# Optimization experiments

Measured on AMD Instinct MI355X. Metric: run time of the kernel, lower is better.

Reference implementation:

```python
import jax, jax.numpy as jnp
import numpy as np

B, S, D, H = 2, 2048, 512, 8
HD = D // H  # head_dim = 64
LN_EPS = 1e-5


def setup_inputs() -> dict:
    key = jax.random.key(0)
    ks = jax.random.split(key, 12)
    sc = 1.0 / np.sqrt(D)
    inp = {
        'q': jax.random.normal(ks[0], (B, S, D), jnp.float32),
        'k': jax.random.normal(ks[1], (B, S, D), jnp.float32),
        'v': jax.random.normal(ks[2], (B, S, D), jnp.float32),
        # torch.nn.Linear stores weight as [out, in]; y = x @ W.T + b
        'wq': jax.random.normal(ks[3], (D, D), jnp.float32) * sc,
        'bq': jnp.zeros((D,), jnp.float32),
        'wk': jax.random.normal(ks[4], (D, D), jnp.float32) * sc,
        'bk': jnp.zeros((D,), jnp.float32),
        'wv': jax.random.normal(ks[5], (D, D), jnp.float32) * sc,
        'bv': jnp.zeros((D,), jnp.float32),
        'wo': jax.random.normal(ks[6], (D, D), jnp.float32) * sc,
        'bo': jnp.zeros((D,), jnp.float32),
        'gamma': jnp.ones((D,), jnp.float32),
        'beta': jnp.zeros((D,), jnp.float32),
        # causal mask: True above the diagonal -> filled with -inf
        'mask': jnp.broadcast_to(jnp.triu(jnp.ones((S, S), bool), k=1)[None, None], (B, 1, S, S)),
    }
    return inp


def _split_heads(x):
    # [B,S,D] -> [B,H,S,HD]
    return x.reshape(B, S, H, HD).transpose(0, 2, 1, 3)


def reference(q, k, v, wq, bq, wk, bk, wv, bv, wo, bo, gamma, beta, mask):
    residual = q
    Q = _split_heads(q @ wq.T + bq)
    K = _split_heads(k @ wk.T + bk)
    V = _split_heads(v @ wv.T + bv)
    scale = jnp.sqrt(jnp.float32(HD)) + 1e-8
    score = jnp.einsum('bhqd,bhkd->bhqk', Q, K) / scale
    score = jnp.where(mask, -jnp.inf, score)
    attn = jax.nn.softmax(score, axis=-1)
    ctx = jnp.einsum('bhqk,bhkd->bhqd', attn, V)
    ctx = ctx.transpose(0, 2, 1, 3).reshape(B, S, D)  # merge heads
    o = ctx @ wo.T + bo  # dropout is identity in eval mode
    x = residual + o
    mu = jnp.mean(x, axis=-1, keepdims=True)
    var = jnp.mean(jnp.square(x - mu), axis=-1, keepdims=True)
    return gamma * (x - mu) * jax.lax.rsqrt(var + LN_EPS) + beta
```

## Files before the change

### kernel.cpp

```cpp
#include <hip/hip_runtime.h>
#include <hip/hip_bf16.h>
#include <math.h>

#define BB 2
#define SS 2048
#define DD 512
#define HH 8
#define HD 64
#define LN_EPS 1e-5f

typedef _Float16 f16;
typedef f16 half8 __attribute__((ext_vector_type(8)));
typedef f16 half4 __attribute__((ext_vector_type(4)));
typedef __fp16 fp16x2 __attribute__((ext_vector_type(2)));

typedef float f32x4 __attribute__((ext_vector_type(4)));

__device__ __forceinline__ half4 cvt4(const float4 v) {
    const fp16x2 p0 = __builtin_amdgcn_cvt_pkrtz(v.x, v.y);
    const fp16x2 p1 = __builtin_amdgcn_cvt_pkrtz(v.z, v.w);
    half4 h;
    h.x = (f16)p0.x; h.y = (f16)p0.y; h.z = (f16)p1.x; h.w = (f16)p1.y;
    return h;
}

__global__ __launch_bounds__(128) void gemm_qkv(
    const float* __restrict__ qin, const float* __restrict__ kin,
    const float* __restrict__ vin,
    const float* __restrict__ wq, const float* __restrict__ wk,
    const float* __restrict__ wv,
    const float* __restrict__ bq, const float* __restrict__ bk,
    const float* __restrict__ bv,
    f16* __restrict__ Qh, f16* __restrict__ Kh, f16* __restrict__ Vt) {
    __shared__ f16 As[128][72];
    __shared__ f16 Bs[64][72];

    const int z = blockIdx.z;
    const float* A;  const float* W;  const float* bias;  f16* out;
    if (z == 0)      { A = qin; W = wq; bias = bq; out = Qh; }
    else if (z == 1) { A = kin; W = wk; bias = bk; out = Kh; }
    else             { A = vin; W = wv; bias = bv; out = Vt; }

    const int tid = threadIdx.x;
    const int lane = tid & 63;
    const int wid = tid >> 6;
    const int m0 = blockIdx.y * 128;
    const int n0 = blockIdx.x * 64;

    const int lr = tid >> 4;
    const int lc = (tid & 15) * 4;

    const int cl = lane & 15;
    const int g  = lane >> 4;

    f32x4 acc[4][4] = {};

    for (int k0 = 0; k0 < DD; k0 += 64) {
#pragma unroll
        for (int p = 0; p < 16; ++p) {
            const int r = p * 8 + lr;
            const float4 v = *reinterpret_cast<const float4*>(A + (size_t)(m0 + r) * DD + k0 + lc);
            *reinterpret_cast<half4*>(&As[r][lc]) = cvt4(v);
        }
#pragma unroll
        for (int p = 0; p < 8; ++p) {
            const int r = p * 8 + lr;
            const float4 v = *reinterpret_cast<const float4*>(W + (size_t)(n0 + r) * DD + k0 + lc);
            *reinterpret_cast<half4*>(&Bs[r][lc]) = cvt4(v);
        }
        __syncthreads();

#pragma unroll
        for (int ks = 0; ks < 2; ++ks) {
            const int co = ks * 32 + g * 8;
            half8 a[4], b[4];
#pragma unroll
            for (int i = 0; i < 4; ++i)
                a[i] = *reinterpret_cast<const half8*>(&As[wid * 64 + i * 16 + cl][co]);
#pragma unroll
            for (int j = 0; j < 4; ++j)
                b[j] = *reinterpret_cast<const half8*>(&Bs[j * 16 + cl][co]);
#pragma unroll
            for (int i = 0; i < 4; ++i)
#pragma unroll
                for (int j = 0; j < 4; ++j)
                    acc[i][j] = __builtin_amdgcn_mfma_f32_16x16x32_f16(a[i], b[j], acc[i][j], 0, 0, 0);
        }
        __syncthreads();
    }

    const int h = n0 >> 6;
#pragma unroll
    for (int i = 0; i < 4; ++i) {
#pragma unroll
        for (int r = 0; r < 4; ++r) {
            const int m = m0 + wid * 64 + i * 16 + g * 4 + r;
            const int b = m >> 11;
            const int s = m & (SS - 1);
#pragma unroll
            for (int j = 0; j < 4; ++j) {
                const int n = n0 + j * 16 + cl;
                const f16 y = (f16)(acc[i][j][r] + bias[n]);
                if (z == 2)
                    out[(((size_t)b * HH + h) * HD + (n & 63)) * SS + s] = y;
                else
                    out[(((size_t)b * HH + h) * SS + s) * HD + (n & 63)] = y;
            }
        }
    }
}

__global__ __launch_bounds__(256) void flash_f16(const f16* __restrict__ Qh,
                                                 const f16* __restrict__ Kh,
                                                 const f16* __restrict__ Vt,
                                                 float* __restrict__ Oc) {
    __shared__ f16 Ks[128][72];
    __shared__ f16 Vs[64][136];
    __shared__ f16 Ps[4][16][136];

    const int tid = threadIdx.x;
    const int lane = tid & 63;
    const int w = tid >> 6;
    const int qt = blockIdx.x;
    const int bh = blockIdx.y;
    const int cl = lane & 15;
    const int g  = lane >> 4;

    const f16* Qb = Qh + (size_t)bh * SS * HD;
    const f16* Kb = Kh + (size_t)bh * SS * HD;
    const f16* Vb = Vt + (size_t)bh * HD * SS;

    const int q0w = qt * 64 + w * 16;

    const f16 qsc = (f16)(0.125f * 1.44269504088896f);
    half8 aq[2];
#pragma unroll
    for (int ks = 0; ks < 2; ++ks) {
        half8 t = *reinterpret_cast<const half8*>(Qb + (size_t)(q0w + cl) * HD + ks * 32 + g * 8);
#pragma unroll
        for (int e = 0; e < 8; ++e) t[e] = t[e] * qsc;
        aq[ks] = t;
    }

    f32x4 ctx[4] = {};
    float m_i[4], l_i[4];
#pragma unroll
    for (int r = 0; r < 4; ++r) { m_i[r] = -INFINITY; l_i[r] = 0.f; }

    const int nfull = (qt * 64) >> 7;

    for (int kt = 0; kt <= nfull; ++kt) {
        const int kvb = kt * 128;
        const bool diag = (kt == nfull);

#pragma unroll
        for (int i = 0; i < 4; ++i) {
            const int c = tid + 256 * i;
            const int kr = c >> 3;
            const int kc = (c & 7) * 8;
            *reinterpret_cast<half8*>(&Ks[kr][kc]) =
                *reinterpret_cast<const half8*>(Kb + (size_t)(kvb + kr) * HD + kc);
            const int vr = c >> 4;
            const int vc = (c & 15) * 8;
            *reinterpret_cast<half8*>(&Vs[vr][vc]) =
                *reinterpret_cast<const half8*>(Vb + (size_t)vr * SS + kvb + vc);
        }
        __syncthreads();

        f32x4 s[8] = {};
#pragma unroll
        for (int ks = 0; ks < 2; ++ks) {
#pragma unroll
            for (int j = 0; j < 8; ++j) {
                const half8 bk = *reinterpret_cast<const half8*>(&Ks[j * 16 + cl][ks * 32 + g * 8]);
                s[j] = __builtin_amdgcn_mfma_f32_16x16x32_f16(aq[ks], bk, s[j], 0, 0, 0);
            }
        }

        if (diag) {
#pragma unroll
            for (int j = 0; j < 8; ++j)
#pragma unroll
                for (int r = 0; r < 4; ++r)
                    if (kvb + j * 16 + cl > q0w + g * 4 + r) s[j][r] = -INFINITY;
        }

#pragma unroll
        for (int r = 0; r < 4; ++r) {
            float mx = s[0][r];
#pragma unroll
            for (int j = 1; j < 8; ++j) mx = fmaxf(mx, s[j][r]);
#pragma unroll
            for (int off = 1; off < 16; off <<= 1) mx = fmaxf(mx, __shfl_xor(mx, off, 16));
            const float newm = fmaxf(m_i[r], mx);
            const float fac = exp2f(m_i[r] - newm);
            float rs = 0.f;
#pragma unroll
            for (int j = 0; j < 8; ++j) {
                const float p = exp2f(s[j][r] - newm);
                s[j][r] = p;
                rs += p;
            }
#pragma unroll
            for (int off = 1; off < 16; off <<= 1) rs += __shfl_xor(rs, off, 16);
            l_i[r] = l_i[r] * fac + rs;
            m_i[r] = newm;
#pragma unroll
            for (int j = 0; j < 4; ++j) ctx[j][r] *= fac;
        }

#pragma unroll
        for (int j = 0; j < 8; ++j)
#pragma unroll
            for (int r = 0; r < 4; ++r)
                Ps[w][g * 4 + r][j * 16 + cl] = (f16)s[j][r];

        half8 ap[4];
#pragma unroll
        for (int ks = 0; ks < 4; ++ks)
            ap[ks] = *reinterpret_cast<const half8*>(&Ps[w][cl][ks * 32 + g * 8]);

#pragma unroll
        for (int ks = 0; ks < 4; ++ks) {
#pragma unroll
            for (int j = 0; j < 4; ++j) {
                const half8 bv = *reinterpret_cast<const half8*>(&Vs[j * 16 + cl][ks * 32 + g * 8]);
                ctx[j] = __builtin_amdgcn_mfma_f32_16x16x32_f16(ap[ks], bv, ctx[j], 0, 0, 0);
            }
        }
        __syncthreads();
    }

    const int b = bh >> 3;
    const int h = bh & (HH - 1);
#pragma unroll
    for (int r = 0; r < 4; ++r) {
        const float inv = 1.0f / l_i[r];
        const int qg = q0w + g * 4 + r;
#pragma unroll
        for (int j = 0; j < 4; ++j)
            Oc[((size_t)b * SS + qg) * DD + h * HD + j * 16 + cl] = ctx[j][r] * inv;
    }
}

__global__ __launch_bounds__(128) void gemm_o(const float* __restrict__ A,
                                              const float* __restrict__ W,
                                              const float* __restrict__ bias,
                                              const float* __restrict__ resid,
                                              float* __restrict__ out) {
    __shared__ f16 As[128][72];
    __shared__ f16 Bs[64][72];

    const int tid = threadIdx.x;
    const int lane = tid & 63;
    const int wid = tid >> 6;
    const int m0 = blockIdx.y * 128;
    const int n0 = blockIdx.x * 64;
    const int lr = tid >> 4;
    const int lc = (tid & 15) * 4;
    const int cl = lane & 15;
    const int g  = lane >> 4;

    f32x4 acc[4][4] = {};

    for (int k0 = 0; k0 < DD; k0 += 64) {
#pragma unroll
        for (int p = 0; p < 16; ++p) {
            const int r = p * 8 + lr;
            const float4 v = *reinterpret_cast<const float4*>(A + (size_t)(m0 + r) * DD + k0 + lc);
            *reinterpret_cast<half4*>(&As[r][lc]) = cvt4(v);
        }
#pragma unroll
        for (int p = 0; p < 8; ++p) {
            const int r = p * 8 + lr;
            const float4 v = *reinterpret_cast<const float4*>(W + (size_t)(n0 + r) * DD + k0 + lc);
            *reinterpret_cast<half4*>(&Bs[r][lc]) = cvt4(v);
        }
        __syncthreads();

#pragma unroll
        for (int ks = 0; ks < 2; ++ks) {
            const int co = ks * 32 + g * 8;
            half8 a[4], b[4];
#pragma unroll
            for (int i = 0; i < 4; ++i)
                a[i] = *reinterpret_cast<const half8*>(&As[wid * 64 + i * 16 + cl][co]);
#pragma unroll
            for (int j = 0; j < 4; ++j)
                b[j] = *reinterpret_cast<const half8*>(&Bs[j * 16 + cl][co]);
#pragma unroll
            for (int i = 0; i < 4; ++i)
#pragma unroll
                for (int j = 0; j < 4; ++j)
                    acc[i][j] = __builtin_amdgcn_mfma_f32_16x16x32_f16(a[i], b[j], acc[i][j], 0, 0, 0);
        }
        __syncthreads();
    }

#pragma unroll
    for (int i = 0; i < 4; ++i) {
#pragma unroll
        for (int r = 0; r < 4; ++r) {
            const int m = m0 + wid * 64 + i * 16 + g * 4 + r;
#pragma unroll
            for (int j = 0; j < 4; ++j) {
                const int n = n0 + j * 16 + cl;
                const size_t idx = (size_t)m * DD + n;
                out[idx] = acc[i][j][r] + bias[n] + resid[idx];
            }
        }
    }
}

__global__ __launch_bounds__(256) void ln_k(const float* __restrict__ X,
                                            const float* __restrict__ gamma,
                                            const float* __restrict__ beta,
                                            float* __restrict__ out) {
    const int row = blockIdx.x * 4 + (threadIdx.x >> 6);
    const int lane = threadIdx.x & 63;
    const float* x = X + (size_t)row * DD;

    const float4 v0 = *reinterpret_cast<const float4*>(x + lane * 4);
    const float4 v1 = *reinterpret_cast<const float4*>(x + 256 + lane * 4);

    float sum = v0.x + v0.y + v0.z + v0.w + v1.x + v1.y + v1.z + v1.w;
#pragma unroll
    for (int off = 1; off < 64; off <<= 1) sum += __shfl_xor(sum, off, 64);
    const float mu = sum * (1.0f / DD);

    const float d0[8] = {v0.x - mu, v0.y - mu, v0.z - mu, v0.w - mu,
                         v1.x - mu, v1.y - mu, v1.z - mu, v1.w - mu};
    float vs = 0.f;
#pragma unroll
    for (int t = 0; t < 8; ++t) vs += d0[t] * d0[t];
#pragma unroll
    for (int off = 1; off < 64; off <<= 1) vs += __shfl_xor(vs, off, 64);
    const float rstd = rsqrtf(vs * (1.0f / DD) + LN_EPS);

    const float4 g0 = *reinterpret_cast<const float4*>(gamma + lane * 4);
    const float4 g1 = *reinterpret_cast<const float4*>(gamma + 256 + lane * 4);
    const float4 b0 = *reinterpret_cast<const float4*>(beta + lane * 4);
    const float4 b1 = *reinterpret_cast<const float4*>(beta + 256 + lane * 4);

    float4 o0, o1;
    o0.x = g0.x * d0[0] * rstd + b0.x;
    o0.y = g0.y * d0[1] * rstd + b0.y;
    o0.z = g0.z * d0[2] * rstd + b0.z;
    o0.w = g0.w * d0[3] * rstd + b0.w;
    o1.x = g1.x * d0[4] * rstd + b1.x;
    o1.y = g1.y * d0[5] * rstd + b1.y;
    o1.z = g1.z * d0[6] * rstd + b1.z;
    o1.w = g1.w * d0[7] * rstd + b1.w;

    *reinterpret_cast<float4*>(out + (size_t)row * DD + lane * 4) = o0;
    *reinterpret_cast<float4*>(out + (size_t)row * DD + 256 + lane * 4) = o1;
}

extern "C" void kernel_launch(void* const* d_in, const int* in_sizes, int n_in,
                              void* d_out, int out_size, void* d_ws, size_t ws_size,
                              hipStream_t stream) {
    const float* q     = (const float*)d_in[0];
    const float* k     = (const float*)d_in[1];
    const float* v     = (const float*)d_in[2];
    const float* wq    = (const float*)d_in[3];
    const float* bq    = (const float*)d_in[4];
    const float* wk    = (const float*)d_in[5];
    const float* bk    = (const float*)d_in[6];
    const float* wv    = (const float*)d_in[7];
    const float* bv    = (const float*)d_in[8];
    const float* wo    = (const float*)d_in[9];
    const float* bo    = (const float*)d_in[10];
    const float* gamma = (const float*)d_in[11];
    const float* beta  = (const float*)d_in[12];

    char* ws = (char*)d_ws;
    f16*   Qh = (f16*)(ws);
    f16*   Kh = (f16*)(ws + (4u << 20));
    f16*   Vt = (f16*)(ws + (8u << 20));
    float* Oc = (float*)(ws + (12u << 20));
    float* X  = (float*)(ws);

    gemm_qkv<<<dim3(DD / 64, (BB * SS) / 128, 3), 128, 0, stream>>>(
        q, k, v, wq, wk, wv, bq, bk, bv, Qh, Kh, Vt);

    flash_f16<<<dim3(SS / 64, BB * HH), 256, 0, stream>>>(Qh, Kh, Vt, Oc);

    gemm_o<<<dim3(DD / 64, (BB * SS) / 128), 128, 0, stream>>>(Oc, wo, bo, q, X);

    ln_k<<<(BB * SS) / 4, 256, 0, stream>>>(X, gamma, beta, (float*)d_out);
}
```

Measured before the change: 246.3 us.

## Pre-convert weights to fp16, retile GEMMs, prefetch KV and transpose flash attention

Adds a kernel that converts all four weight matrices to fp16 once per call, so the GEMMs load fp16 weights directly. The QKV GEMM now uses 128x128 tiles with 4 waves, and the output GEMM uses 256 threads. Flash attention computes S^T, so the softmax reduction needs only cross-group shuffles. It register-prefetches the next K/V tile during compute and writes the context in fp16 instead of fp32, halving that intermediate's traffic. This adds an extra launch and some fp16 rounding of the attention output in exchange.

New measurement: 212.8 us. 13.6% less time.

```diff
diff --git a/kernel.cpp b/kernel.cpp
--- a/kernel.cpp
+++ b/kernel.cpp
@@ -13,7 +13,6 @@
 typedef f16 half8 __attribute__((ext_vector_type(8)));
 typedef f16 half4 __attribute__((ext_vector_type(4)));
 typedef __fp16 fp16x2 __attribute__((ext_vector_type(2)));
-
 typedef float f32x4 __attribute__((ext_vector_type(4)));
 
 __device__ __forceinline__ half4 cvt4(const float4 v) {
@@ -24,62 +23,70 @@
     return h;
 }
 
-__global__ __launch_bounds__(128) void gemm_qkv(
+__global__ __launch_bounds__(256) void cvt_w(const float* __restrict__ a, const float* __restrict__ b,
+                                             const float* __restrict__ c, const float* __restrict__ d,
+                                             f16* __restrict__ oa, f16* __restrict__ ob,
+                                             f16* __restrict__ oc, f16* __restrict__ od) {
+    const int i = blockIdx.x * 256 + threadIdx.x;
+    ((half4*)oa)[i] = cvt4(((const float4*)a)[i]);
+    ((half4*)ob)[i] = cvt4(((const float4*)b)[i]);
+    ((half4*)oc)[i] = cvt4(((const float4*)c)[i]);
+    ((half4*)od)[i] = cvt4(((const float4*)d)[i]);
+}
+
+__global__ __launch_bounds__(256) void gemm_qkv(
     const float* __restrict__ qin, const float* __restrict__ kin,
     const float* __restrict__ vin,
-    const float* __restrict__ wq, const float* __restrict__ wk,
-    const float* __restrict__ wv,
+    const f16* __restrict__ wqf, const f16* __restrict__ wkf,
+    const f16* __restrict__ wvf,
     const float* __restrict__ bq, const float* __restrict__ bk,
     const float* __restrict__ bv,
     f16* __restrict__ Qh, f16* __restrict__ Kh, f16* __restrict__ Vt) {
     __shared__ f16 As[128][72];
-    __shared__ f16 Bs[64][72];
+    __shared__ f16 Bs[128][72];
 
     const int z = blockIdx.z;
-    const float* A;  const float* W;  const float* bias;  f16* out;
-    if (z == 0)      { A = qin; W = wq; bias = bq; out = Qh; }
-    else if (z == 1) { A = kin; W = wk; bias = bk; out = Kh; }
-    else             { A = vin; W = wv; bias = bv; out = Vt; }
+    const float* A; const f16* W; const float* bias; f16* out;
+    if (z == 0)      { A = qin; W = wqf; bias = bq; out = Qh; }
+    else if (z == 1) { A = kin; W = wkf; bias = bk; out = Kh; }
+    else             { A = vin; W = wvf; bias = bv; out = Vt; }
 
     const int tid = threadIdx.x;
     const int lane = tid & 63;
     const int wid = tid >> 6;
-    const int m0 = blockIdx.y * 128;
-    const int n0 = blockIdx.x * 64;
-
-    const int lr = tid >> 4;
-    const int lc = (tid & 15) * 4;
-
-    const int cl = lane & 15;
-    const int g  = lane >> 4;
+    const int wr = wid >> 1, wc = wid & 1;
+    const int cl = lane & 15, g = lane >> 4;
+    const int m0 = blockIdx.y * 128, n0 = blockIdx.x * 128;
+    const int srow = tid >> 1, scp = tid & 1;
 
     f32x4 acc[4][4] = {};
 
     for (int k0 = 0; k0 < DD; k0 += 64) {
 #pragma unroll
-        for (int p = 0; p < 16; ++p) {
-            const int r = p * 8 + lr;
-            const float4 v = *reinterpret_cast<const float4*>(A + (size_t)(m0 + r) * DD + k0 + lc);
-            *reinterpret_cast<half4*>(&As[r][lc]) = cvt4(v);
-        }
-#pragma unroll
-        for (int p = 0; p < 8; ++p) {
-            const int r = p * 8 + lr;
-            const float4 v = *reinterpret_cast<const float4*>(W + (size_t)(n0 + r) * DD + k0 + lc);
-            *reinterpret_cast<half4*>(&Bs[r][lc]) = cvt4(v);
-        }
+        for (int p = 0; p < 4; ++p) {
+            const float* src = A + (size_t)(m0 + srow) * DD + k0 + scp * 32 + p * 8;
+            const half4 lo = cvt4(*(const float4*)src);
+            const half4 hi = cvt4(*(const float4*)(src + 4));
+            half8 h;
+            h[0]=lo.x; h[1]=lo.y; h[2]=lo.z; h[3]=lo.w;
+            h[4]=hi.x; h[5]=hi.y; h[6]=hi.z; h[7]=hi.w;
+            *(half8*)&As[srow][scp * 32 + p * 8] = h;
+        }
+#pragma unroll
+        for (int p = 0; p < 4; ++p)
+            *(half8*)&Bs[srow][scp * 32 + p * 8] =
+                *(const half8*)(W + (size_t)(n0 + srow) * DD + k0 + scp * 32 + p * 8);
         __syncthreads();
 
 #pragma unroll
         for (int ks = 0; ks < 2; ++ks) {
-            const int co = ks * 32 + g * 8;
             half8 a[4], b[4];
 #pragma unroll
             for (int i = 0; i < 4; ++i)
-                a[i] = *reinterpret_cast<const half8*>(&As[wid * 64 + i * 16 + cl][co]);
+                a[i] = *(const half8*)&As[wr * 64 + i * 16 + cl][ks * 32 + g * 8];
 #pragma unroll
             for (int j = 0; j < 4; ++j)
-                b[j] = *reinterpret_cast<const half8*>(&Bs[j * 16 + cl][co]);
+                b[j] = *(const half8*)&Bs[wc * 64 + j * 16 + cl][ks * 32 + g * 8];
 #pragma unroll
             for (int i = 0; i < 4; ++i)
 #pragma unroll
@@ -89,22 +96,20 @@
         __syncthreads();
     }
 
-    const int h = n0 >> 6;
-#pragma unroll
-    for (int i = 0; i < 4; ++i) {
-#pragma unroll
-        for (int r = 0; r < 4; ++r) {
-            const int m = m0 + wid * 64 + i * 16 + g * 4 + r;
-            const int b = m >> 11;
-            const int s = m & (SS - 1);
-#pragma unroll
-            for (int j = 0; j < 4; ++j) {
-                const int n = n0 + j * 16 + cl;
-                const f16 y = (f16)(acc[i][j][r] + bias[n]);
-                if (z == 2)
-                    out[(((size_t)b * HH + h) * HD + (n & 63)) * SS + s] = y;
-                else
-                    out[(((size_t)b * HH + h) * SS + s) * HD + (n & 63)] = y;
+#pragma unroll
+    for (int j = 0; j < 4; ++j) {
+        const int n = n0 + wc * 64 + j * 16 + cl;
+        const int h = n >> 6, d = n & 63;
+        const float bn = bias[n];
+#pragma unroll
+        for (int i = 0; i < 4; ++i) {
+#pragma unroll
+            for (int r = 0; r < 4; ++r) {
+                const int m = m0 + wr * 64 + i * 16 + g * 4 + r;
+                const int b = m >> 11, s = m & (SS - 1);
+                const f16 y = (f16)(acc[i][j][r] + bn);
+                if (z == 2) out[(((size_t)b * HH + h) * HD + d) * SS + s] = y;
+                else        out[(((size_t)b * HH + h) * SS + s) * HD + d] = y;
             }
         }
     }
@@ -113,7 +118,7 @@
 __global__ __launch_bounds__(256) void flash_f16(const f16* __restrict__ Qh,
                                                  const f16* __restrict__ Kh,
                                                  const f16* __restrict__ Vt,
-                                                 float* __restrict__ Oc) {
+                                                 f16* __restrict__ Of) {
     __shared__ f16 Ks[128][72];
     __shared__ f16 Vs[64][136];
     __shared__ f16 Ps[4][16][136];
@@ -123,128 +128,149 @@
     const int w = tid >> 6;
     const int qt = blockIdx.x;
     const int bh = blockIdx.y;
-    const int cl = lane & 15;
-    const int g  = lane >> 4;
+    const int cl = lane & 15, g = lane >> 4;
 
     const f16* Qb = Qh + (size_t)bh * SS * HD;
     const f16* Kb = Kh + (size_t)bh * SS * HD;
     const f16* Vb = Vt + (size_t)bh * HD * SS;
 
     const int q0w = qt * 64 + w * 16;
+    const int qlane = q0w + cl;
 
     const f16 qsc = (f16)(0.125f * 1.44269504088896f);
-    half8 aq[2];
+    half8 bq[2];
 #pragma unroll
     for (int ks = 0; ks < 2; ++ks) {
-        half8 t = *reinterpret_cast<const half8*>(Qb + (size_t)(q0w + cl) * HD + ks * 32 + g * 8);
+        half8 t = *(const half8*)(Qb + (size_t)qlane * HD + ks * 32 + g * 8);
 #pragma unroll
         for (int e = 0; e < 8; ++e) t[e] = t[e] * qsc;
-        aq[ks] = t;
-    }
-
-    f32x4 ctx[4] = {};
-    float m_i[4], l_i[4];
-#pragma unroll
-    for (int r = 0; r < 4; ++r) { m_i[r] = -INFINITY; l_i[r] = 0.f; }
+        bq[ks] = t;
+    }
+
+    f32x4 ctxT[4] = {};
+    float m_s = -INFINITY, l_s = 0.f;
 
     const int nfull = (qt * 64) >> 7;
+
+    half8 kreg[4], vreg[4];
+#define LOADT(KT)                                                                     \
+    {                                                                                 \
+        const int kvbase = (KT) * 128;                                                \
+        _Pragma("unroll") for (int i2 = 0; i2 < 4; ++i2) {                            \
+            const int c = tid + 256 * i2;                                             \
+            kreg[i2] = *(const half8*)(Kb + (size_t)(kvbase + (c >> 3)) * HD + (c & 7) * 8); \
+            vreg[i2] = *(const half8*)(Vb + (size_t)(c >> 4) * SS + kvbase + (c & 15) * 8);  \
+        }                                                                             \
+    }
+#define WRITET()                                                                      \
+    {                                                                                 \
+        _Pragma("unroll") for (int i2 = 0; i2 < 4; ++i2) {                            \
+            const int c = tid + 256 * i2;                                             \
+            *(half8*)&Ks[c >> 3][(c & 7) * 8] = kreg[i2];                             \
+            *(half8*)&Vs[c >> 4][(c & 15) * 8] = vreg[i2];                            \
+        }                                                                             \
+    }
+
+    LOADT(0);
+    WRITET();
+    __syncthreads();
 
     for (int kt = 0; kt <= nfull; ++kt) {
         const int kvb = kt * 128;
         const bool diag = (kt == nfull);
 
-#pragma unroll
-        for (int i = 0; i < 4; ++i) {
-            const int c = tid + 256 * i;
-            const int kr = c >> 3;
-            const int kc = (c & 7) * 8;
-            *reinterpret_cast<half8*>(&Ks[kr][kc]) =
-                *reinterpret_cast<const half8*>(Kb + (size_t)(kvb + kr) * HD + kc);
-            const int vr = c >> 4;
-            const int vc = (c & 15) * 8;
-            *reinterpret_cast<half8*>(&Vs[vr][vc]) =
-                *reinterpret_cast<const half8*>(Vb + (size_t)vr * SS + kvb + vc);
-        }
-        __syncthreads();
+        if (kt < nfull) LOADT(kt + 1);
 
         f32x4 s[8] = {};
 #pragma unroll
         for (int ks = 0; ks < 2; ++ks) {
 #pragma unroll
             for (int j = 0; j < 8; ++j) {
-                const half8 bk = *reinterpret_cast<const half8*>(&Ks[j * 16 + cl][ks * 32 + g * 8]);
-                s[j] = __builtin_amdgcn_mfma_f32_16x16x32_f16(aq[ks], bk, s[j], 0, 0, 0);
+                const half8 ak = *(const half8*)&Ks[j * 16 + cl][ks * 32 + g * 8];
+                s[j] = __builtin_amdgcn_mfma_f32_16x16x32_f16(ak, bq[ks], s[j], 0, 0, 0);
             }
         }
 
         if (diag) {
 #pragma unroll
-            for (int j = 0; j < 8; ++j)
+            for (int j = 0; j < 8; ++j) {
+                const int kvj = kvb + j * 16 + g * 4;
 #pragma unroll
                 for (int r = 0; r < 4; ++r)
-                    if (kvb + j * 16 + cl > q0w + g * 4 + r) s[j][r] = -INFINITY;
-        }
-
-#pragma unroll
-        for (int r = 0; r < 4; ++r) {
-            float mx = s[0][r];
-#pragma unroll
-            for (int j = 1; j < 8; ++j) mx = fmaxf(mx, s[j][r]);
-#pragma unroll
-            for (int off = 1; off < 16; off <<= 1) mx = fmaxf(mx, __shfl_xor(mx, off, 16));
-            const float newm = fmaxf(m_i[r], mx);
-            const float fac = exp2f(m_i[r] - newm);
-            float rs = 0.f;
-#pragma unroll
-            for (int j = 0; j < 8; ++j) {
+                    if (kvj + r > qlane) s[j][r] = -INFINITY;
+            }
+        }
+
+        float mx = -INFINITY;
+#pragma unroll
+        for (int j = 0; j < 8; ++j)
+            mx = fmaxf(mx, fmaxf(fmaxf(s[j][0], s[j][1]), fmaxf(s[j][2], s[j][3])));
+        mx = fmaxf(mx, __shfl_xor(mx, 16));
+        mx = fmaxf(mx, __shfl_xor(mx, 32));
+
+        const float newm = fmaxf(m_s, mx);
+        const float fac = exp2f(m_s - newm);
+        float rs = 0.f;
+#pragma unroll
+        for (int j = 0; j < 8; ++j) {
+#pragma unroll
+            for (int r = 0; r < 4; ++r) {
                 const float p = exp2f(s[j][r] - newm);
                 s[j][r] = p;
                 rs += p;
             }
-#pragma unroll
-            for (int off = 1; off < 16; off <<= 1) rs += __shfl_xor(rs, off, 16);
-            l_i[r] = l_i[r] * fac + rs;
-            m_i[r] = newm;
-#pragma unroll
-            for (int j = 0; j < 4; ++j) ctx[j][r] *= fac;
-        }
-
-#pragma unroll
-        for (int j = 0; j < 8; ++j)
-#pragma unroll
-            for (int r = 0; r < 4; ++r)
-                Ps[w][g * 4 + r][j * 16 + cl] = (f16)s[j][r];
-
-        half8 ap[4];
+        }
+        rs += __shfl_xor(rs, 16);
+        rs += __shfl_xor(rs, 32);
+        l_s = l_s * fac + rs;
+        m_s = newm;
+#pragma unroll
+        for (int jj = 0; jj < 4; ++jj) ctxT[jj] *= fac;
+
+#pragma unroll
+        for (int j = 0; j < 8; ++j) {
+            half4 t;
+            t.x = (f16)s[j][0]; t.y = (f16)s[j][1]; t.z = (f16)s[j][2]; t.w = (f16)s[j][3];
+            *(half4*)&Ps[w][cl][j * 16 + g * 4] = t;
+        }
+
+        half8 bp[4];
 #pragma unroll
         for (int ks = 0; ks < 4; ++ks)
-            ap[ks] = *reinterpret_cast<const half8*>(&Ps[w][cl][ks * 32 + g * 8]);
+            bp[ks] = *(const half8*)&Ps[w][cl][ks * 32 + g * 8];
 
 #pragma unroll
         for (int ks = 0; ks < 4; ++ks) {
 #pragma unroll
-            for (int j = 0; j < 4; ++j) {
-                const half8 bv = *reinterpret_cast<const half8*>(&Vs[j * 16 + cl][ks * 32 + g * 8]);
-                ctx[j] = __builtin_amdgcn_mfma_f32_16x16x32_f16(ap[ks], bv, ctx[j], 0, 0, 0);
-            }
-        }
-        __syncthreads();
-    }
+            for (int jj = 0; jj < 4; ++jj) {
+                const half8 av = *(const half8*)&Vs[jj * 16 + cl][ks * 32 + g * 8];
+                ctxT[jj] = __builtin_amdgcn_mfma_f32_16x16x32_f16(av, bp[ks], ctxT[jj], 0, 0, 0);
+            }
+        }
+
+        __syncthreads();
+        if (kt < nfull) { WRITET(); }
+        __syncthreads();
+    }
+#undef LOADT
+#undef WRITET
 
     const int b = bh >> 3;
     const int h = bh & (HH - 1);
-#pragma unroll
-    for (int r = 0; r < 4; ++r) {
-        const float inv = 1.0f / l_i[r];
-        const int qg = q0w + g * 4 + r;
-#pragma unroll
-        for (int j = 0; j < 4; ++j)
-            Oc[((size_t)b * SS + qg) * DD + h * HD + j * 16 + cl] = ctx[j][r] * inv;
-    }
-}
-
-__global__ __launch_bounds__(128) void gemm_o(const float* __restrict__ A,
-                                              const float* __restrict__ W,
+    const float inv = 1.0f / l_s;
+#pragma unroll
+    for (int jj = 0; jj < 4; ++jj) {
+        half4 o;
+        o.x = (f16)(ctxT[jj][0] * inv);
+        o.y = (f16)(ctxT[jj][1] * inv);
+        o.z = (f16)(ctxT[jj][2] * inv);
+        o.w = (f16)(ctxT[jj][3] * inv);
+        *(half4*)&Of[((size_t)b * SS + qlane) * DD + h * HD + jj * 16 + g * 4] = o;
+    }
+}
+
+__global__ __launch_bounds__(256) void gemm_o(const f16* __restrict__ A,
+                                              const f16* __restrict__ W,
                                               const float* __restrict__ bias,
                                               const float* __restrict__ resid,
                                               float* __restrict__ out) {
@@ -254,59 +280,56 @@
     const int tid = threadIdx.x;
     const int lane = tid & 63;
     const int wid = tid >> 6;
-    const int m0 = blockIdx.y * 128;
-    const int n0 = blockIdx.x * 64;
-    const int lr = tid >> 4;
-    const int lc = (tid & 15) * 4;
-    const int cl = lane & 15;
-    const int g  = lane >> 4;
-
-    f32x4 acc[4][4] = {};
+    const int wr = wid >> 1, wc = wid & 1;
+    const int cl = lane & 15, g = lane >> 4;
+    const int m0 = blockIdx.y * 128, n0 = blockIdx.x * 64;
+
+    f32x4 acc[4][2] = {};
 
     for (int k0 = 0; k0 < DD; k0 += 64) {
-#pragma unroll
-        for (int p = 0; p < 16; ++p) {
-            const int r = p * 8 + lr;
-            const float4 v = *reinterpret_cast<const float4*>(A + (size_t)(m0 + r) * DD + k0 + lc);
-            *reinterpret_cast<half4*>(&As[r][lc]) = cvt4(v);
-        }
-#pragma unroll
-        for (int p = 0; p < 8; ++p) {
-            const int r = p * 8 + lr;
-            const float4 v = *reinterpret_cast<const float4*>(W + (size_t)(n0 + r) * DD + k0 + lc);
-            *reinterpret_cast<half4*>(&Bs[r][lc]) = cvt4(v);
+        {
+            const int srow = tid >> 1, scp = tid & 1;
+#pragma unroll
+            for (int p = 0; p < 4; ++p)
+                *(half8*)&As[srow][scp * 32 + p * 8] =
+                    *(const half8*)(A + (size_t)(m0 + srow) * DD + k0 + scp * 32 + p * 8);
+            const int brow = tid >> 2, bcq = tid & 3;
+#pragma unroll
+            for (int p = 0; p < 2; ++p)
+                *(half8*)&Bs[brow][bcq * 16 + p * 8] =
+                    *(const half8*)(W + (size_t)(n0 + brow) * DD + k0 + bcq * 16 + p * 8);
         }
         __syncthreads();
 
 #pragma unroll
         for (int ks = 0; ks < 2; ++ks) {
-            const int co = ks * 32 + g * 8;
-            half8 a[4], b[4];
+            half8 a[4], b[2];
 #pragma unroll
             for (int i = 0; i < 4; ++i)
-                a[i] = *reinterpret_cast<const half8*>(&As[wid * 64 + i * 16 + cl][co]);
-#pragma unroll
-            for (int j = 0; j < 4; ++j)
-                b[j] = *reinterpret_cast<const half8*>(&Bs[j * 16 + cl][co]);
+                a[i] = *(const half8*)&As[wr * 64 + i * 16 + cl][ks * 32 + g * 8];
+#pragma unroll
+            for (int j = 0; j < 2; ++j)
+                b[j] = *(const half8*)&Bs[wc * 32 + j * 16 + cl][ks * 32 + g * 8];
 #pragma unroll
             for (int i = 0; i < 4; ++i)
 #pragma unroll
-                for (int j = 0; j < 4; ++j)
+                for (int j = 0; j < 2; ++j)
                     acc[i][j] = __builtin_amdgcn_mfma_f32_16x16x32_f16(a[i], b[j], acc[i][j], 0, 0, 0);
         }
         __syncthreads();
     }
 
 #pragma unroll
-    for (int i = 0; i < 4; ++i) {
-#pragma unroll
-        for (int r = 0; r < 4; ++r) {
-            const int m = m0 + wid * 64 + i * 16 + g * 4 + r;
-#pragma unroll
-            for (int j = 0; j < 4; ++j) {
-                const int n = n0 + j * 16 + cl;
+    for (int j = 0; j < 2; ++j) {
+        const int n = n0 + wc * 32 + j * 16 + cl;
+        const float bn = bias[n];
+#pragma unroll
+        for (int i = 0; i < 4; ++i) {
+#pragma unroll
+            for (int r = 0; r < 4; ++r) {
+                const int m = m0 + wr * 64 + i * 16 + g * 4 + r;
                 const size_t idx = (size_t)m * DD + n;
-                out[idx] = acc[i][j][r] + bias[n] + resid[idx];
+                out[idx] = acc[i][j][r] + bn + resid[idx];
             }
         }
     }
@@ -374,18 +397,25 @@
     const float* beta  = (const float*)d_in[12];
 
     char* ws = (char*)d_ws;
-    f16*   Qh = (f16*)(ws);
-    f16*   Kh = (f16*)(ws + (4u << 20));
-    f16*   Vt = (f16*)(ws + (8u << 20));
-    float* Oc = (float*)(ws + (12u << 20));
-    float* X  = (float*)(ws);
-
-    gemm_qkv<<<dim3(DD / 64, (BB * SS) / 128, 3), 128, 0, stream>>>(
-        q, k, v, wq, wk, wv, bq, bk, bv, Qh, Kh, Vt);
-
-    flash_f16<<<dim3(SS / 64, BB * HH), 256, 0, stream>>>(Qh, Kh, Vt, Oc);
-
-    gemm_o<<<dim3(DD / 64, (BB * SS) / 128), 128, 0, stream>>>(Oc, wo, bo, q, X);
+    const size_t MB = 1u << 20;
+    f16*   Qh  = (f16*)(ws);
+    f16*   Kh  = (f16*)(ws + 4 * MB);
+    f16*   Vt  = (f16*)(ws + 8 * MB);
+    f16*   Of  = (f16*)(ws + 12 * MB);
+    f16*   wqf = (f16*)(ws + 16 * MB);
+    f16*   wkf = (f16*)(ws + 16 * MB + 512 * 1024);
+    f16*   wvf = (f16*)(ws + 17 * MB);
+    f16*   wof = (f16*)(ws + 17 * MB + 512 * 1024);
+    float* X   = (float*)(ws);
+
+    cvt_w<<<256, 256, 0, stream>>>(wq, wk, wv, wo, wqf, wkf, wvf, wof);
+
+    gemm_qkv<<<dim3(4, 32, 3), 256, 0, stream>>>(
+        q, k, v, wqf, wkf, wvf, bq, bk, bv, Qh, Kh, Vt);
+
+    flash_f16<<<dim3(SS / 64, BB * HH), 256, 0, stream>>>(Qh, Kh, Vt, Of);
+
+    gemm_o<<<dim3(8, 32), 256, 0, stream>>>(Of, wof, bo, q, X);
 
     ln_k<<<(BB * SS) / 4, 256, 0, stream>>>(X, gamma, beta, (float*)d_out);
 }
```
